# Performance work log

Measured on AMD Instinct MI355X. Metric: run time of the kernel, lower is better.

## Reference

```python
import jax, jax.numpy as jnp
import numpy as np

N = 50000
E = 800000
IN_C, HID_C, OUT_C = 128, 256, 2


def sage_conv(x, src, dst, W_l, b_l, W_r, num_nodes):
    # PyG SAGEConv with mean aggregation:
    #   out = lin_l(mean_{j in N(i)} x_j) + lin_r(x_i)
    msg = x[src]                                            # [E, d] gather
    agg = jax.ops.segment_sum(msg, dst, num_segments=num_nodes)   # [N, d]
    cnt = jax.ops.segment_sum(jnp.ones((msg.shape[0],), x.dtype), dst,
                              num_segments=num_nodes)        # [N]
    agg = agg / jnp.maximum(cnt, 1.0)[:, None]               # mean (deg>=1)
    return agg @ W_l.T + b_l + x @ W_r.T


def setup_inputs() -> dict:
    key = jax.random.key(0)
    ks = jax.random.split(key, 8)
    x = jax.random.normal(ks[0], (N, IN_C), dtype=jnp.float32)
    edge_index = jax.random.randint(ks[1], (2, E), 0, N, dtype=jnp.int32)
    # glorot-ish scaled params
    s1 = 1.0 / np.sqrt(IN_C)
    s2 = 1.0 / np.sqrt(HID_C)
    W1l = jax.random.normal(ks[2], (HID_C, IN_C), dtype=jnp.float32) * s1
    W1r = jax.random.normal(ks[3], (HID_C, IN_C), dtype=jnp.float32) * s1
    b1 = jnp.zeros((HID_C,), dtype=jnp.float32)
    W2l = jax.random.normal(ks[4], (OUT_C, HID_C), dtype=jnp.float32) * s2
    W2r = jax.random.normal(ks[5], (OUT_C, HID_C), dtype=jnp.float32) * s2
    b2 = jnp.zeros((OUT_C,), dtype=jnp.float32)
    return {"x": x, "edge_index": edge_index,
            "W1l": W1l, "b1": b1, "W1r": W1r,
            "W2l": W2l, "b2": b2, "W2r": W2r}


def reference(x, edge_index, W1l, b1, W1r, W2l, b2, W2r):
    src, dst = edge_index[0], edge_index[1]
    h = sage_conv(x, src, dst, W1l, b1, W1r, N)
    h = jax.nn.relu(h)
    out = sage_conv(h, src, dst, W2l, b2, W2r, N)
    return out
```

## Files before the change

kernel.cpp:

```cpp
#include <hip/hip_runtime.h>
#include <hip/hip_bf16.h>


#define IN_C 128
#define HID_C 256
#define BKT_SHIFT 7
#define BKT_W 128
#define CAP 3072

typedef __attribute__((ext_vector_type(8))) short short8;
typedef __attribute__((ext_vector_type(4))) float f32x4;

static __device__ __forceinline__ unsigned short f2b(float f) {
    __hip_bfloat16 h = __float2bfloat16(f);
    return *(unsigned short*)&h;
}
static __device__ __forceinline__ float b2f(unsigned short u) {
    unsigned v = ((unsigned)u) << 16;
    return *(float*)&v;
}

__global__ __launch_bounds__(512) void scatter_conv(
    const float* __restrict__ x, unsigned int* __restrict__ Abf,
    const float* __restrict__ w1l, const float* __restrict__ w1r,
    unsigned short* __restrict__ Bg,
    const int* __restrict__ ei, int* __restrict__ bcnt,
    unsigned int* __restrict__ binned,
    int nquads , int xblk, int E_) {
    __shared__ int hist[512];
    __shared__ int lbase[512];
    const int tid = threadIdx.x;
    if (blockIdx.x < xblk) {
        int t = blockIdx.x * 512 + tid;
        if (t >= nquads) return;
        float4 v = *(const float4*)&x[(size_t)t * 4];
        uint2 o;
        o.x = ((unsigned)f2b(v.y) << 16) | f2b(v.x);
        o.y = ((unsigned)f2b(v.w) << 16) | f2b(v.z);
        int node = t >> 5, g = t & 31;
        *(uint2*)&Abf[(size_t)node * 128 + 64 + g * 2] = o;
    } else if (blockIdx.x < xblk + 32) {
        int idx4 = (blockIdx.x - xblk) * 512 + tid;
        int o = idx4 >> 6, k4 = (idx4 & 63) * 4;
        const float* srcp = (k4 < IN_C) ? &w1l[o * IN_C + k4]
                                        : &w1r[o * IN_C + (k4 - IN_C)];
        float4 f = *(const float4*)srcp;
        ushort4 s;
        s.x = f2b(f.x); s.y = f2b(f.y); s.z = f2b(f.z); s.w = f2b(f.w);
        *(ushort4*)&Bg[(size_t)idx4 * 4] = s;
    } else {
        const int e0 = (blockIdx.x - xblk - 32) * 2048;
        hist[tid] = 0;
        __syncthreads();
        int dreg[4];
#pragma unroll
        for (int j = 0; j < 4; ++j) {
            int e = e0 + j * 512 + tid;
            dreg[j] = (e < E_) ? ei[E_ + e] : -1;
            if (dreg[j] >= 0) atomicAdd(&hist[dreg[j] >> BKT_SHIFT], 1);
        }
        __syncthreads();
        {
            int c = hist[tid];
            lbase[tid] = c ? tid * CAP + atomicAdd(&bcnt[tid], c) : 0;
            hist[tid] = 0;
        }
        __syncthreads();
#pragma unroll
        for (int j = 0; j < 4; ++j) {
            int e = e0 + j * 512 + tid;
            if (dreg[j] >= 0) {
                int d = dreg[j];
                int b = d >> BKT_SHIFT;
                int pos = lbase[b] + atomicAdd(&hist[b], 1);
                if (pos < b * CAP + CAP)
                    binned[pos] = ((unsigned)ei[e] << BKT_SHIFT) |
                                  (unsigned)(d & (BKT_W - 1));
            }
        }
    }
}


__global__ __launch_bounds__(1024) void sort_gather(
    unsigned int* __restrict__ binned, const int* __restrict__ bcnt,
    const uint4* __restrict__ abf4c, uint4* __restrict__ Abf4,
    int* __restrict__ deg, int* __restrict__ boffs, int n) {
    __shared__ unsigned int ebuf[CAP];
    __shared__ unsigned short sbuf[CAP];
    __shared__ int hist[BKT_W];
    __shared__ int offs[BKT_W];
    __shared__ int cur[BKT_W];
    const int tid = threadIdx.x;
    const int lane = tid & 63;
    const int bkt = blockIdx.x;
    const int gbase = bkt * CAP;
    int cnt = bcnt[bkt];
    if (cnt > CAP) cnt = CAP;

    if (tid < BKT_W) hist[tid] = 0;
    {
        const int cnt4 = cnt >> 2;
        const uint4* b4 = (const uint4*)(binned + gbase);
        uint4* e4 = (uint4*)ebuf;
        for (int i = tid; i < cnt4; i += 1024) e4[i] = b4[i];
        for (int i = cnt4 * 4 + tid; i < cnt; i += 1024)
            ebuf[i] = binned[gbase + i];
    }
    __syncthreads();
    for (int i = tid; i < cnt; i += 1024)
        atomicAdd(&hist[ebuf[i] & (BKT_W - 1)], 1);
    __syncthreads();
    if (tid < 64) {
        int h0 = hist[lane * 2], h1 = hist[lane * 2 + 1];
        int s = h0 + h1;
        int incl = s;
#pragma unroll
        for (int off = 1; off < 64; off <<= 1) {
            int t = __shfl_up(incl, off);
            if (lane >= off) incl += t;
        }
        int excl = incl - s;
        offs[lane * 2] = excl;          cur[lane * 2] = excl;
        offs[lane * 2 + 1] = excl + h0; cur[lane * 2 + 1] = excl + h0;
    }
    __syncthreads();
    for (int i = tid; i < cnt; i += 1024) {
        unsigned int pk = ebuf[i];
        int pos = atomicAdd(&cur[pk & (BKT_W - 1)], 1);
        sbuf[pos] = (unsigned short)(pk >> BKT_SHIFT);
    }
    if (tid < BKT_W) {
        int node = bkt * BKT_W + tid;
        if (node < n) { deg[node] = hist[tid]; boffs[node] = offs[tid]; }
    }
    __syncthreads();

    {
        unsigned int* so = (unsigned int*)(binned + gbase);
        const int half = (cnt + 1) >> 1;
        for (int i = tid; i < half; i += 1024) {
            unsigned lo = sbuf[i * 2];
            unsigned hi = (i * 2 + 1 < cnt) ? sbuf[i * 2 + 1] : 0u;
            so[i] = lo | (hi << 16);
        }
    }

    const int wv = tid >> 6;
    const int ep = lane >> 4;
    const int pos = lane & 15;
    for (int ld = wv * 8; ld < wv * 8 + 8; ++ld) {
        int node = bkt * BKT_W + ld;
        if (node >= n) break;
        int beg = offs[ld], end = offs[ld] + hist[ld];
        float s[8] = {0.f, 0.f, 0.f, 0.f, 0.f, 0.f, 0.f, 0.f};
        for (int e = beg; e < end; e += 16) {
#pragma unroll
            for (int g = 0; g < 4; ++g) {
                int eg = e + g * 4 + ep;
                if (eg < end) {
                    int src = sbuf[eg];
                    uint4 u = abf4c[(size_t)src * 32 + 16 + pos];
                    s[0] += b2f(u.x & 0xffff); s[1] += b2f(u.x >> 16);
                    s[2] += b2f(u.y & 0xffff); s[3] += b2f(u.y >> 16);
                    s[4] += b2f(u.z & 0xffff); s[5] += b2f(u.z >> 16);
                    s[6] += b2f(u.w & 0xffff); s[7] += b2f(u.w >> 16);
                }
            }
        }
#pragma unroll
        for (int i = 0; i < 8; ++i) {
            s[i] += __shfl_xor(s[i], 16);
            s[i] += __shfl_xor(s[i], 32);
        }
        if (ep == 0) {
            float inv = 1.0f / (float)max(end - beg, 1);
            uint4 o;
            o.x = ((unsigned)f2b(s[1] * inv) << 16) | f2b(s[0] * inv);
            o.y = ((unsigned)f2b(s[3] * inv) << 16) | f2b(s[2] * inv);
            o.z = ((unsigned)f2b(s[5] * inv) << 16) | f2b(s[4] * inv);
            o.w = ((unsigned)f2b(s[7] * inv) << 16) | f2b(s[6] * inv);
            Abf4[(size_t)node * 32 + pos] = o;
        }
    }
}


#define LSTR 72

__global__ __launch_bounds__(256) void gemm1_fused(
    const unsigned short* __restrict__ Abf, const unsigned short* __restrict__ Bg,
    const float* __restrict__ b1, const float* __restrict__ w2l,
    const float* __restrict__ w2r, float* __restrict__ p2g,
    float* __restrict__ rsg, int nn, int full16) {
    __shared__ short As[128 * LSTR];
    __shared__ short Bs[128 * LSTR];

    int idx = blockIdx.x;
    int rowt, colt;
    if (idx < full16) {
        int g = idx >> 4, r = idx & 15;
        rowt = g * 8 + (r & 7);
        colt = r >> 3;
    } else {
        int r2 = idx - full16;
        rowt = (full16 >> 1) + (r2 >> 1);
        colt = r2 & 1;
    }
    const int row0 = rowt * 128;
    const int col0 = colt * 128;

    const int tid = threadIdx.x;
    const int lane = tid & 63;
    const int wid = tid >> 6;
    const int wm = wid >> 1, wn = wid & 1;

    const int srow = tid >> 1;
    const int skc = (tid & 1) * 32;
    int arow = row0 + srow;
    if (arow >= nn) arow = nn - 1;
    const size_t agoff = (size_t)arow * 256 + skc;
    const size_t bgoff = (size_t)(col0 + srow) * 256 + skc;

    f32x4 acc[4][4];
#pragma unroll
    for (int i = 0; i < 4; ++i)
#pragma unroll
        for (int j = 0; j < 4; ++j) acc[i][j] = (f32x4){0.f, 0.f, 0.f, 0.f};

    const int quad = lane >> 4;
    const int l16 = lane & 15;

    uint4 va0, va1, va2, va3, vb0, vb1, vb2, vb3;
    {
        const uint4* ga = (const uint4*)(Abf + agoff);
        const uint4* gb = (const uint4*)(Bg + bgoff);
        va0 = ga[0]; va1 = ga[1]; va2 = ga[2]; va3 = ga[3];
        vb0 = gb[0]; vb1 = gb[1]; vb2 = gb[2]; vb3 = gb[3];
    }

    for (int k0 = 0; k0 < 256; k0 += 64) {
        __syncthreads();
        uint4* la = (uint4*)&As[srow * LSTR + skc];
        uint4* lb = (uint4*)&Bs[srow * LSTR + skc];
        la[0] = va0; la[1] = va1; la[2] = va2; la[3] = va3;
        lb[0] = vb0; lb[1] = vb1; lb[2] = vb2; lb[3] = vb3;
        __syncthreads();

        if (k0 + 64 < 256) {
            const uint4* ga = (const uint4*)(Abf + agoff + k0 + 64);
            const uint4* gb = (const uint4*)(Bg + bgoff + k0 + 64);
            va0 = ga[0]; va1 = ga[1]; va2 = ga[2]; va3 = ga[3];
            vb0 = gb[0]; vb1 = gb[1]; vb2 = gb[2]; vb3 = gb[3];
        }

#pragma unroll
        for (int kb = 0; kb < 2; ++kb) {
            short8 af[4], bf[4];
#pragma unroll
            for (int mt = 0; mt < 4; ++mt)
                af[mt] = *(const short8*)&As[(wm * 64 + mt * 16 + l16) * LSTR + kb * 32 + quad * 8];
#pragma unroll
            for (int nt = 0; nt < 4; ++nt)
                bf[nt] = *(const short8*)&Bs[(wn * 64 + nt * 16 + l16) * LSTR + kb * 32 + quad * 8];
#pragma unroll
            for (int mt = 0; mt < 4; ++mt)
#pragma unroll
                for (int nt = 0; nt < 4; ++nt)
                    acc[mt][nt] = __builtin_amdgcn_mfma_f32_16x16x32_bf16(
                        af[mt], bf[nt], acc[mt][nt], 0, 0, 0);
        }
    }

    const int cbase = col0 + wn * 64 + l16;
#pragma unroll
    for (int half = 0; half < 2; ++half) {
        const float* wA = half ? w2r : w2l;
        float* og = half ? rsg : p2g;
        f32x4 part[2][4];
#pragma unroll
        for (int c = 0; c < 2; ++c)
#pragma unroll
            for (int mt = 0; mt < 4; ++mt) part[c][mt] = (f32x4){0.f, 0.f, 0.f, 0.f};
#pragma unroll
        for (int nt = 0; nt < 4; ++nt) {
            const int col = cbase + nt * 16;
            const float bias = b1[col];
            const float w0 = wA[col];
            const float w1 = wA[HID_C + col];
#pragma unroll
            for (int mt = 0; mt < 4; ++mt)
#pragma unroll
                for (int r = 0; r < 4; ++r) {
                    float hv = fmaxf(acc[mt][nt][r] + bias, 0.0f);
                    part[0][mt][r] += hv * w0;
                    part[1][mt][r] += hv * w1;
                }
        }
#pragma unroll
        for (int c = 0; c < 2; ++c)
#pragma unroll
            for (int mt = 0; mt < 4; ++mt)
#pragma unroll
                for (int r = 0; r < 4; ++r)
#pragma unroll
                    for (int m = 1; m < 16; m <<= 1)
                        part[c][mt][r] += __shfl_xor(part[c][mt][r], m);
        if (l16 < 8) {
            const int ch2 = l16 & 1;
            const int mts = l16 >> 1;
#pragma unroll
            for (int r = 0; r < 4; ++r) {
                int row = row0 + wm * 64 + quad * 4 + mts * 16 + r;
                if (row < nn)
                    atomicAdd(&og[row * 2 + ch2], part[ch2][mts][r]);
            }
        }
    }
}


__global__ __launch_bounds__(512) void fin_bucket(
    const unsigned int* __restrict__ binned, const int* __restrict__ boffs,
    const int* __restrict__ deg,
    const float2* __restrict__ p2, const float2* __restrict__ rs,
    const float* __restrict__ b2, float* __restrict__ out, int n) {
    __shared__ float ps0[3][BKT_W];
    __shared__ float ps1[3][BKT_W];
    const int tid = threadIdx.x;
    const int ln = tid & (BKT_W - 1);
    const int hp = tid >> 7;
    const int bkt = blockIdx.x;
    const int node = bkt * BKT_W + ln;
    const unsigned short* sp =
        (const unsigned short*)(binned + (size_t)bkt * CAP);
    float s0 = 0.f, s1 = 0.f;
    int dg = 0;
    if (node < n) {
        int beg = boffs[node];
        dg = deg[node];
        int end = beg + dg;
        for (int i = beg + hp; i < end; i += 4) {
            float2 v = p2[sp[i]];
            s0 += v.x; s1 += v.y;
        }
    }
    if (hp) { ps0[hp - 1][ln] = s0; ps1[hp - 1][ln] = s1; }
    __syncthreads();
    if (!hp && node < n) {
        s0 += ps0[0][ln] + ps0[1][ln] + ps0[2][ln];
        s1 += ps1[0][ln] + ps1[1][ln] + ps1[2][ln];
        float inv = 1.0f / (float)max(dg, 1);
        float2 self = rs[node];
        out[node * 2 + 0] = s0 * inv + self.x + b2[0];
        out[node * 2 + 1] = s1 * inv + self.y + b2[1];
    }
}


extern "C" void kernel_launch(void* const* d_in, const int* in_sizes, int n_in,
                              void* d_out, int out_size, void* d_ws, size_t ws_size,
                              hipStream_t stream) {
    const float* x   = (const float*)d_in[0];
    const int*   ei  = (const int*)d_in[1];
    const float* W1l = (const float*)d_in[2];
    const float* b1  = (const float*)d_in[3];
    const float* W1r = (const float*)d_in[4];
    const float* W2l = (const float*)d_in[5];
    const float* b2  = (const float*)d_in[6];
    const float* W2r = (const float*)d_in[7];
    float* out = (float*)d_out;

    const int N_ = in_sizes[0] / IN_C;
    const int E_ = in_sizes[1] / 2;
    const int nbkt = (N_ + BKT_W - 1) / BKT_W;

    char* wsb = (char*)d_ws;
    size_t off = 0;
    auto alloc = [&](size_t bytes) {
        void* ptr = wsb + off;
        off += ((bytes + 15) & ~(size_t)15);
        return ptr;
    };
    unsigned short* Abf = (unsigned short*)alloc((size_t)N_ * 256 * 2);
    unsigned short* Bg  = (unsigned short*)alloc(256 * 256 * 2);
    unsigned int* binned = (unsigned int*)alloc((size_t)(nbkt + 1) * CAP * 4);
    int*   bcnt = (int*)alloc(512 * 4);
    float* p2f  = (float*)alloc((size_t)N_ * 2 * 4);
    float* rsf  = (float*)alloc((size_t)N_ * 2 * 4);
    int*   deg  = (int*)alloc((size_t)N_ * 4);
    int*   boffs = (int*)alloc((size_t)N_ * 4);

    const int xblk = (N_ * 32 + 511) / 512;
    const int eblk = (E_ + 2047) / 2048;

    hipMemsetAsync(bcnt, 0, 512 * sizeof(int) + (size_t)N_ * 2 * 4 * 2, stream);

    scatter_conv<<<xblk + 32 + eblk, 512, 0, stream>>>(
        x, (unsigned int*)Abf, W1l, W1r, Bg, ei, bcnt, binned,
        N_ * 32, xblk, E_);

    sort_gather<<<nbkt, 1024, 0, stream>>>(binned, bcnt, (const uint4*)Abf,
                                           (uint4*)Abf, deg, boffs, N_);

    const int nbx = (N_ + 127) / 128;
    const int full16 = (nbx / 8) * 16;
    gemm1_fused<<<nbx * 2, 256, 0, stream>>>(
        Abf, Bg, b1, W2l, W2r, p2f, rsf, N_, full16);

    fin_bucket<<<nbkt, 512, 0, stream>>>(binned, boffs, deg,
                                         (const float2*)p2f, (const float2*)rsf,
                                         b2, out, N_);
}
```

Baseline: 191.2 us.

## Load MFMA fragments directly from global memory in gemm1, dropping LDS staging

The first-layer GEMM kernel no longer stages A and B tiles through shared memory with barriers and a register prefetch. Each lane now reads its bf16 MFMA fragments straight from global memory, relying on L1/L2 caching for reuse across waves. The grouped block-index swizzle is replaced by a plain 2D grid, and launch bounds now request higher occupancy. The aim is to remove LDS traffic and synchronization, at the cost of less coalesced global loads and weaker L2 locality. The row clamp for the last partial tile is gone, so those rows may read past the end of Abf unless the buffer is padded.

```diff
diff --git a/kernel.cpp b/kernel.cpp
--- a/kernel.cpp
+++ b/kernel.cpp
@@ -186,90 +186,54 @@
 }
 
 
-#define LSTR 72
-
-__global__ __launch_bounds__(256) void gemm1_fused(
+__global__ __launch_bounds__(256, 4) void gemm1_fused(
     const unsigned short* __restrict__ Abf, const unsigned short* __restrict__ Bg,
     const float* __restrict__ b1, const float* __restrict__ w2l,
     const float* __restrict__ w2r, float* __restrict__ p2g,
-    float* __restrict__ rsg, int nn, int full16) {
-    __shared__ short As[128 * LSTR];
-    __shared__ short Bs[128 * LSTR];
-
-    int idx = blockIdx.x;
-    int rowt, colt;
-    if (idx < full16) {
-        int g = idx >> 4, r = idx & 15;
-        rowt = g * 8 + (r & 7);
-        colt = r >> 3;
-    } else {
-        int r2 = idx - full16;
-        rowt = (full16 >> 1) + (r2 >> 1);
-        colt = r2 & 1;
-    }
-    const int row0 = rowt * 128;
-    const int col0 = colt * 128;
-
+    float* __restrict__ rsg, int nn) {
     const int tid = threadIdx.x;
     const int lane = tid & 63;
     const int wid = tid >> 6;
     const int wm = wid >> 1, wn = wid & 1;
-
-    const int srow = tid >> 1;
-    const int skc = (tid & 1) * 32;
-    int arow = row0 + srow;
-    if (arow >= nn) arow = nn - 1;
-    const size_t agoff = (size_t)arow * 256 + skc;
-    const size_t bgoff = (size_t)(col0 + srow) * 256 + skc;
-
-    f32x4 acc[4][4];
-#pragma unroll
-    for (int i = 0; i < 4; ++i)
-#pragma unroll
-        for (int j = 0; j < 4; ++j) acc[i][j] = (f32x4){0.f, 0.f, 0.f, 0.f};
-
+    const int row0 = blockIdx.x * 128;
+    const int col0 = blockIdx.y * 128;
     const int quad = lane >> 4;
     const int l16 = lane & 15;
 
-    uint4 va0, va1, va2, va3, vb0, vb1, vb2, vb3;
-    {
-        const uint4* ga = (const uint4*)(Abf + agoff);
-        const uint4* gb = (const uint4*)(Bg + bgoff);
-        va0 = ga[0]; va1 = ga[1]; va2 = ga[2]; va3 = ga[3];
-        vb0 = gb[0]; vb1 = gb[1]; vb2 = gb[2]; vb3 = gb[3];
-    }
-
-    for (int k0 = 0; k0 < 256; k0 += 64) {
-        __syncthreads();
-        uint4* la = (uint4*)&As[srow * LSTR + skc];
-        uint4* lb = (uint4*)&Bs[srow * LSTR + skc];
-        la[0] = va0; la[1] = va1; la[2] = va2; la[3] = va3;
-        lb[0] = vb0; lb[1] = vb1; lb[2] = vb2; lb[3] = vb3;
-        __syncthreads();
-
-        if (k0 + 64 < 256) {
-            const uint4* ga = (const uint4*)(Abf + agoff + k0 + 64);
-            const uint4* gb = (const uint4*)(Bg + bgoff + k0 + 64);
-            va0 = ga[0]; va1 = ga[1]; va2 = ga[2]; va3 = ga[3];
-            vb0 = gb[0]; vb1 = gb[1]; vb2 = gb[2]; vb3 = gb[3];
-        }
-
-#pragma unroll
-        for (int kb = 0; kb < 2; ++kb) {
-            short8 af[4], bf[4];
-#pragma unroll
-            for (int mt = 0; mt < 4; ++mt)
-                af[mt] = *(const short8*)&As[(wm * 64 + mt * 16 + l16) * LSTR + kb * 32 + quad * 8];
+    const unsigned short* ap[4];
+#pragma unroll
+    for (int mt = 0; mt < 4; ++mt) {
+        int ar = row0 + wm * 64 + mt * 16 + l16;
+        ap[mt] = Abf + (size_t)ar * 256 + quad * 8;
+    }
+    const unsigned short* bp[4];
+#pragma unroll
+    for (int nt = 0; nt < 4; ++nt) {
+        int bc = col0 + wn * 64 + nt * 16 + l16;
+        bp[nt] = Bg + (size_t)bc * 256 + quad * 8;
+    }
+
+    f32x4 acc[4][4];
+#pragma unroll
+    for (int i = 0; i < 4; ++i)
+#pragma unroll
+        for (int j = 0; j < 4; ++j) acc[i][j] = (f32x4){0.f, 0.f, 0.f, 0.f};
+
+#pragma unroll 2
+    for (int ks = 0; ks < 8; ++ks) {
+        short8 af[4], bf[4];
+#pragma unroll
+        for (int mt = 0; mt < 4; ++mt)
+            af[mt] = *(const short8*)(ap[mt] + ks * 32);
+#pragma unroll
+        for (int nt = 0; nt < 4; ++nt)
+            bf[nt] = *(const short8*)(bp[nt] + ks * 32);
+#pragma unroll
+        for (int mt = 0; mt < 4; ++mt)
 #pragma unroll
             for (int nt = 0; nt < 4; ++nt)
-                bf[nt] = *(const short8*)&Bs[(wn * 64 + nt * 16 + l16) * LSTR + kb * 32 + quad * 8];
-#pragma unroll
-            for (int mt = 0; mt < 4; ++mt)
-#pragma unroll
-                for (int nt = 0; nt < 4; ++nt)
-                    acc[mt][nt] = __builtin_amdgcn_mfma_f32_16x16x32_bf16(
-                        af[mt], bf[nt], acc[mt][nt], 0, 0, 0);
-        }
+                acc[mt][nt] = __builtin_amdgcn_mfma_f32_16x16x32_bf16(
+                    af[mt], bf[nt], acc[mt][nt], 0, 0, 0);
     }
 
     const int cbase = col0 + wn * 64 + l16;
@@ -403,10 +367,8 @@
     sort_gather<<<nbkt, 1024, 0, stream>>>(binned, bcnt, (const uint4*)Abf,
                                            (uint4*)Abf, deg, boffs, N_);
 
-    const int nbx = (N_ + 127) / 128;
-    const int full16 = (nbx / 8) * 16;
-    gemm1_fused<<<nbx * 2, 256, 0, stream>>>(
-        Abf, Bg, b1, W2l, W2r, p2f, rsf, N_, full16);
+    gemm1_fused<<<dim3((N_ + 127) / 128, 2), 256, 0, stream>>>(
+        Abf, Bg, b1, W2l, W2r, p2f, rsf, N_);
 
     fin_bucket<<<nbkt, 512, 0, stream>>>(binned, boffs, deg,
                                          (const float2*)p2f, (const float2*)rsf,
```

Result: slower. 209.6 us (+9.6%).
